# Kernel tuning notes

Hardware: AMD Instinct MI355X
Metric: run time of the kernel (lower is better)

Reference implementation:

```python
import jax, jax.numpy as jnp
import numpy as np

S, N, F = 32, 512, 256        # systems, atoms per system, feature/charge channels
R_EXCL = 5.0                  # neighbor_list_options.cutoff -> exclusion_radius
BOX = 30.0                    # box edge for random positions (Angstrom-scale)


def setup_inputs() -> dict:
    key = jax.random.key(0)
    k1, k2, k3, k4 = jax.random.split(key, 4)
    positions = jax.random.uniform(k1, (S, N, 3), dtype=jnp.float32) * BOX
    features = jax.random.normal(k2, (S * N, F), dtype=jnp.float32)
    W = jax.random.normal(k3, (F, F), dtype=jnp.float32) / jnp.sqrt(F)
    b = jax.random.normal(k4, (F,), dtype=jnp.float32) * 0.01
    return {"positions": positions, "features": features, "W": W, "b": b}


def _pair_potential(d):
    # CoulombPotential(smearing=None, exclusion_radius=R_EXCL).from_dist:
    # v(r) = (1/r) * (1 - f_cut(r)),  f_cut = 0.5*(1 + cos(pi*r/R_EXCL)) for r < R_EXCL
    fcut = jnp.where(d < R_EXCL, 0.5 * (1.0 + jnp.cos(jnp.pi * d / R_EXCL)), 0.0)
    return (1.0 / d) * (1.0 - fcut)


def reference(positions, features, W, b):
    # charges_map: Linear(F, F)
    charges = features @ W.T + b                      # [S*N, F]
    q = charges.reshape(S, N, F)                      # per-system charges

    # all-pairs distances per system (torch.combinations path, both directions
    # accumulated by the half-neighbor-list Calculator)
    diff = positions[:, :, None, :] - positions[:, None, :, :]   # [S,N,N,3]
    d = jnp.sqrt(jnp.sum(diff * diff, axis=-1))                  # [S,N,N]
    eye = jnp.eye(N, dtype=bool)
    d_safe = jnp.where(eye, 1.0, d)
    v = jnp.where(eye, 0.0, _pair_potential(d_safe))             # [S,N,N]

    # V_i = 0.5 * sum_j v(r_ij) q_j  (torchpme energy convention E = sum_i q_i V_i)
    V = 0.5 * jnp.einsum('sij,sjf->sif', v, q)                   # [S,N,F]

    # module returns potential * charges, concatenated over systems
    return (V * q).reshape(S * N, F)
```

## Files before the change

kernel.cpp:

```cpp
#include <hip/hip_runtime.h>
#include <hip/hip_cooperative_groups.h>

#define SY 32
#define NA 512
#define FD 256

typedef __attribute__((ext_vector_type(8))) short bf16x8;
typedef __attribute__((ext_vector_type(4))) short bf16x4;
typedef __attribute__((ext_vector_type(4))) float f32x4;

static __device__ __forceinline__ short f2bf(float x) {
    union { float f; unsigned u; } v; v.f = x;
    unsigned r = v.u + 0x7fffu + ((v.u >> 16) & 1u);
    return (short)(r >> 16);
}
static __device__ __forceinline__ float bf2f(short x) {
    union { float f; unsigned u; } v;
    v.u = ((unsigned)(unsigned short)x) << 16;
    return v.f;
}

static __device__ __forceinline__ void gld16(const void* g, void* l) {
    __builtin_amdgcn_global_load_lds(
        (const __attribute__((address_space(1))) void*)g,
        (__attribute__((address_space(3))) void*)l,
        16, 0, 0);
}

__global__ __launch_bounds__(256, 2) void charges_v2(
    const float* __restrict__ feat, const float* __restrict__ W,
    const float* __restrict__ b, short* __restrict__ qT)
{
    __shared__ __attribute__((aligned(16))) short sA[32 * 72];
    __shared__ __attribute__((aligned(16))) short sB[256 * 72];
    short* tr = sB;
    const int t    = threadIdx.x;
    const int i0   = blockIdx.x * 32;
    const int w    = t >> 6;
    const int lane = t & 63;
    const int n16  = lane & 15;
    const int quad = lane >> 4;

    f32x4 acc[2][4];
    #pragma unroll
    for (int a = 0; a < 2; ++a)
        #pragma unroll
        for (int c = 0; c < 4; ++c) acc[a][c] = (f32x4)0.0f;

    for (int k0 = 0; k0 < FD; k0 += 64) {
        #pragma unroll
        for (int m = 0; m < 2; ++m) {
            int lin = t + 256 * m;
            int i = lin >> 4, kq = lin & 15;
            float4 v = *(const float4*)&feat[(size_t)(i0 + i) * FD + k0 + 4 * kq];
            bf16x4 p; p[0] = f2bf(v.x); p[1] = f2bf(v.y);
                      p[2] = f2bf(v.z); p[3] = f2bf(v.w);
            *(bf16x4*)&sA[i * 72 + 4 * kq] = p;
        }
        #pragma unroll
        for (int m = 0; m < 16; ++m) {
            int lin = t + 256 * m;
            int f = lin >> 4, kq = lin & 15;
            float4 v = *(const float4*)&W[(size_t)f * FD + k0 + 4 * kq];
            bf16x4 p; p[0] = f2bf(v.x); p[1] = f2bf(v.y);
                      p[2] = f2bf(v.z); p[3] = f2bf(v.w);
            *(bf16x4*)&sB[f * 72 + 4 * kq] = p;
        }
        __syncthreads();

        #pragma unroll
        for (int ks = 0; ks < 64; ks += 32) {
            bf16x8 af[2], bfr[4];
            #pragma unroll
            for (int it = 0; it < 2; ++it)
                af[it] = *(const bf16x8*)&sA[(16 * it + n16) * 72 + ks + quad * 8];
            #pragma unroll
            for (int fb = 0; fb < 4; ++fb)
                bfr[fb] = *(const bf16x8*)&sB[(64 * w + 16 * fb + n16) * 72 + ks + quad * 8];
            __builtin_amdgcn_s_setprio(1);
            #pragma unroll
            for (int it = 0; it < 2; ++it)
                #pragma unroll
                for (int fb = 0; fb < 4; ++fb)
                    acc[it][fb] = __builtin_amdgcn_mfma_f32_16x16x32_bf16(
                        af[it], bfr[fb], acc[it][fb], 0, 0, 0);
            __builtin_amdgcn_s_setprio(0);
        }
        __syncthreads();
    }

    float bias[4];
    #pragma unroll
    for (int fb = 0; fb < 4; ++fb) bias[fb] = b[64 * w + 16 * fb + n16];

    #pragma unroll
    for (int it = 0; it < 2; ++it)
        #pragma unroll
        for (int fb = 0; fb < 4; ++fb) {
            bf16x4 p;
            #pragma unroll
            for (int r = 0; r < 4; ++r) p[r] = f2bf(acc[it][fb][r] + bias[fb]);
            int f = 64 * w + 16 * fb + n16;
            *(bf16x4*)&tr[f * 40 + 16 * it + 4 * quad] = p;
        }
    __syncthreads();
    {
        short* qTs = qT + ((size_t)(i0 >> 9)) * FD * NA;
        const int ilb = i0 & 511;
        #pragma unroll
        for (int n = 0; n < 4; ++n) {
            int S = n * 256 + t;
            int f = S >> 2;
            int c = S & 3;
            uint4 v = *(const uint4*)&tr[f * 40 + c * 8];
            *(uint4*)&qTs[(size_t)f * NA + ilb + c * 8] = v;
        }
    }
}

__global__ __launch_bounds__(256, 2) void lr_fast(
    const float* __restrict__ pos, float* __restrict__ gbuf,
    const short* __restrict__ qT)
{
    __shared__ float px[NA], py[NA], pz[NA];
    __shared__ __attribute__((aligned(16))) short sqb[FD * 128];
    __shared__ __attribute__((aligned(16))) short svb[32 * 128];

    const int blk = blockIdx.x;
    const int s   = blk & 31;
    const int i0  = (blk >> 5) * 32;
    const int t   = threadIdx.x;
    const int w    = t >> 6;
    const int lane = t & 63;
    const int n16  = lane & 15;
    const int quad = lane >> 4;

    for (int m = t; m < NA; m += 256) {
        const float* p = &pos[((size_t)s * NA + m) * 3];
        px[m] = p[0]; py[m] = p[1]; pz[m] = p[2];
    }

    f32x4 acc[2][4];
    #pragma unroll
    for (int a = 0; a < 2; ++a)
        #pragma unroll
        for (int c = 0; c < 4; ++c) acc[a][c] = (f32x4)0.0f;
    float qreg[2][4][4];

    const short* qTs = qT + (size_t)s * FD * NA;
    const int pi = t & 31;
    const int pc = t >> 5;
    const int gi = i0 + pi;
    const int wbase = t & ~63;

    __syncthreads();
    const float xi = px[gi], yi = py[gi], zi = pz[gi];

    for (int j0 = 0; j0 < NA; j0 += 128) {
        #pragma unroll
        for (int n = 0; n < 16; ++n) {
            int Sl = n * 256 + t;
            int f  = Sl >> 4;
            int cs = Sl & 15;
            int c  = (cs - f) & 15;
            gld16(&qTs[(size_t)f * NA + j0 + c * 8],
                  &sqb[(n * 256 + wbase) * 8]);
        }
        bf16x8 vA, vB;
        #pragma unroll
        for (int jj = 0; jj < 8; ++jj) {
            int gj = j0 + pc * 16 + jj;
            float dx = xi - px[gj];
            float dy = yi - py[gj];
            float dz = zi - pz[gj];
            float r2 = dx * dx + dy * dy + dz * dz;
            float inv = __builtin_amdgcn_rsqf(r2);
            float dd  = r2 * inv;
            float sn = __sinf(dd * 0.31415926535f);
            float om = (dd < 5.0f) ? sn * sn : 1.0f;
            float vv = (gi != gj) ? 0.5f * om * inv : 0.0f;
            vA[jj] = f2bf(vv);
        }
        #pragma unroll
        for (int jj = 0; jj < 8; ++jj) {
            int gj = j0 + pc * 16 + 8 + jj;
            float dx = xi - px[gj];
            float dy = yi - py[gj];
            float dz = zi - pz[gj];
            float r2 = dx * dx + dy * dy + dz * dz;
            float inv = __builtin_amdgcn_rsqf(r2);
            float dd  = r2 * inv;
            float sn = __sinf(dd * 0.31415926535f);
            float om = (dd < 5.0f) ? sn * sn : 1.0f;
            float vv = (gi != gj) ? 0.5f * om * inv : 0.0f;
            vB[jj] = f2bf(vv);
        }
        *(bf16x8*)&svb[pi * 128 + (((2 * pc + pi) & 15) * 8)]     = vA;
        *(bf16x8*)&svb[pi * 128 + (((2 * pc + 1 + pi) & 15) * 8)] = vB;
        __syncthreads();

        if (j0 == (i0 & ~127)) {
            const int jb0 = i0 & 127;
            #pragma unroll
            for (int it = 0; it < 2; ++it)
                #pragma unroll
                for (int fb = 0; fb < 4; ++fb) {
                    int f = 64 * w + 16 * fb + n16;
                    #pragma unroll
                    for (int r = 0; r < 4; ++r) {
                        int jl = jb0 + 16 * it + 4 * quad + r;
                        int c  = jl >> 3, o = jl & 7;
                        qreg[it][fb][r] =
                            bf2f(sqb[f * 128 + (((c + f) & 15) * 8) + o]);
                    }
                }
        }

        #pragma unroll
        for (int kh = 0; kh < 4; ++kh) {
            const int c = kh * 4 + quad;
            bf16x8 a0 = *(const bf16x8*)&svb[n16 * 128 + (((c + n16) & 15) * 8)];
            bf16x8 a1 = *(const bf16x8*)&svb[(16 + n16) * 128 + (((c + 16 + n16) & 15) * 8)];
            bf16x8 bq[4];
            #pragma unroll
            for (int fb = 0; fb < 4; ++fb) {
                int f = 64 * w + 16 * fb + n16;
                bq[fb] = *(const bf16x8*)&sqb[f * 128 + (((c + f) & 15) * 8)];
            }
            __builtin_amdgcn_s_setprio(1);
            #pragma unroll
            for (int fb = 0; fb < 4; ++fb) {
                acc[0][fb] = __builtin_amdgcn_mfma_f32_16x16x32_bf16(
                    a0, bq[fb], acc[0][fb], 0, 0, 0);
                acc[1][fb] = __builtin_amdgcn_mfma_f32_16x16x32_bf16(
                    a1, bq[fb], acc[1][fb], 0, 0, 0);
            }
            __builtin_amdgcn_s_setprio(0);
        }
        __syncthreads();
    }

    #pragma unroll
    for (int it = 0; it < 2; ++it)
        #pragma unroll
        for (int fb = 0; fb < 4; ++fb)
            #pragma unroll
            for (int r = 0; r < 4; ++r) {
                int i = i0 + 16 * it + 4 * quad + r;
                int f = 64 * w + 16 * fb + n16;
                size_t a = ((size_t)s * NA + i) * FD + f;
                gbuf[a] = acc[it][fb][r] * qreg[it][fb][r];
            }
}

__global__ __launch_bounds__(512) void charges_mfma(
    const float* __restrict__ feat, const float* __restrict__ W,
    const float* __restrict__ b, float* __restrict__ qfp,
    short* __restrict__ qT)
{
    __shared__ __attribute__((aligned(16))) short sA[64 * 72];
    __shared__ __attribute__((aligned(16))) short sB[256 * 72];
    __shared__ __attribute__((aligned(16))) short tr[256 * 72];
    const int t    = threadIdx.x;
    const int i0   = blockIdx.x * 64;
    const int w    = t >> 6;
    const int lane = t & 63;
    const int n16  = lane & 15;
    const int quad = lane >> 4;

    f32x4 acc[4][2];
    #pragma unroll
    for (int a = 0; a < 4; ++a)
        #pragma unroll
        for (int c = 0; c < 2; ++c) acc[a][c] = (f32x4)0.0f;

    for (int k0 = 0; k0 < FD; k0 += 64) {
        #pragma unroll
        for (int m = 0; m < 2; ++m) {
            int lin = t + 512 * m;
            int i = lin >> 4, kq = lin & 15;
            float4 v = *(const float4*)&feat[(size_t)(i0 + i) * FD + k0 + 4 * kq];
            bf16x4 p; p[0] = f2bf(v.x); p[1] = f2bf(v.y);
                      p[2] = f2bf(v.z); p[3] = f2bf(v.w);
            *(bf16x4*)&sA[i * 72 + 4 * kq] = p;
        }
        #pragma unroll
        for (int m = 0; m < 8; ++m) {
            int lin = t + 512 * m;
            int f = lin >> 4, kq = lin & 15;
            float4 v = *(const float4*)&W[(size_t)f * FD + k0 + 4 * kq];
            bf16x4 p; p[0] = f2bf(v.x); p[1] = f2bf(v.y);
                      p[2] = f2bf(v.z); p[3] = f2bf(v.w);
            *(bf16x4*)&sB[f * 72 + 4 * kq] = p;
        }
        __syncthreads();

        #pragma unroll
        for (int ks = 0; ks < 64; ks += 32) {
            bf16x8 af[4], bfr[2];
            #pragma unroll
            for (int it = 0; it < 4; ++it)
                af[it] = *(const bf16x8*)&sA[(16 * it + n16) * 72 + ks + quad * 8];
            #pragma unroll
            for (int fb = 0; fb < 2; ++fb)
                bfr[fb] = *(const bf16x8*)&sB[(32 * w + 16 * fb + n16) * 72 + ks + quad * 8];
            #pragma unroll
            for (int it = 0; it < 4; ++it)
                #pragma unroll
                for (int fb = 0; fb < 2; ++fb)
                    acc[it][fb] = __builtin_amdgcn_mfma_f32_16x16x32_bf16(
                        af[it], bfr[fb], acc[it][fb], 0, 0, 0);
        }
        __syncthreads();
    }

    float bias[2];
    #pragma unroll
    for (int fb = 0; fb < 2; ++fb) bias[fb] = b[32 * w + 16 * fb + n16];

    if (qfp) {
        #pragma unroll
        for (int it = 0; it < 4; ++it)
            #pragma unroll
            for (int fb = 0; fb < 2; ++fb)
                #pragma unroll
                for (int r = 0; r < 4; ++r) {
                    int i = i0 + 16 * it + 4 * quad + r;
                    int f = 32 * w + 16 * fb + n16;
                    qfp[(size_t)i * FD + f] = acc[it][fb][r] + bias[fb];
                }
    }

    #pragma unroll
    for (int it = 0; it < 4; ++it)
        #pragma unroll
        for (int fb = 0; fb < 2; ++fb) {
            bf16x4 p;
            #pragma unroll
            for (int r = 0; r < 4; ++r) p[r] = f2bf(acc[it][fb][r] + bias[fb]);
            int f = 32 * w + 16 * fb + n16;
            *(bf16x4*)&tr[f * 72 + 16 * it + 4 * quad] = p;
        }
    __syncthreads();
    {
        short* qTs = qT + ((size_t)(i0 >> 9)) * FD * NA;
        const int ilb = i0 & 511;
        #pragma unroll
        for (int n = 0; n < 4; ++n) {
            int S = n * 512 + t;
            int f = S >> 3;
            int c = S & 7;
            uint4 v = *(const uint4*)&tr[f * 72 + c * 8];
            *(uint4*)&qTs[(size_t)f * NA + ilb + c * 8] = v;
        }
    }
}

__global__ __launch_bounds__(256) void lr_coop(
    const float* __restrict__ pos, float* __restrict__ gbuf)
{
    __shared__ float px[NA], py[NA], pz[NA];
    __shared__ __attribute__((aligned(16))) short svb[64 * 40];
    __shared__ __attribute__((aligned(16))) short sqb[FD * 40];

    const int blk = blockIdx.x;
    const int s   = blk & 31;
    const int i0  = (blk >> 5) * 64;
    const int t   = threadIdx.x;
    const int w    = t >> 6;
    const int lane = t & 63;
    const int n16  = lane & 15;
    const int quad = lane >> 4;

    for (int m = t; m < NA; m += 256) {
        const float* p = &pos[((size_t)s * NA + m) * 3];
        px[m] = p[0]; py[m] = p[1]; pz[m] = p[2];
    }

    f32x4 acc[4][4];
    #pragma unroll
    for (int a = 0; a < 4; ++a)
        #pragma unroll
        for (int c = 0; c < 4; ++c) acc[a][c] = (f32x4)0.0f;

    __syncthreads();

    const int fq  = t >> 2;
    const int jb  = t & 3;
    const int iv  = t & 63;
    const int jbv = t >> 6;
    const int gi  = i0 + iv;

    float4 rq[8];
    #pragma unroll
    for (int m = 0; m < 8; ++m)
        rq[m] = *(const float4*)&gbuf[((size_t)s * NA + 8 * jb + m) * FD + 4 * fq];

    for (int j0 = 0; j0 < NA; j0 += 32) {
        bf16x8 vrow;
        #pragma unroll
        for (int jj = 0; jj < 8; ++jj) {
            int gj = j0 + 8 * jbv + jj;
            float dx = px[gi] - px[gj];
            float dy = py[gi] - py[gj];
            float dz = pz[gi] - pz[gj];
            float dd = sqrtf(dx * dx + dy * dy + dz * dz);
            float om = (dd < 5.0f) ? 0.5f * (1.0f - __cosf(dd * 0.62831853071795f))
                                   : 1.0f;
            float vv = (gi != gj) ? (0.5f * om * __builtin_amdgcn_rcpf(dd)) : 0.0f;
            vrow[jj] = f2bf(vv);
        }
        bf16x8 rows[4];
        #pragma unroll
        for (int m = 0; m < 8; ++m) {
            rows[0][m] = f2bf(rq[m].x);
            rows[1][m] = f2bf(rq[m].y);
            rows[2][m] = f2bf(rq[m].z);
            rows[3][m] = f2bf(rq[m].w);
        }
        #pragma unroll
        for (int d = 0; d < 4; ++d) {
            int f = 4 * fq + d;
            int phys = (jb + (f >> 3)) & 3;
            *(bf16x8*)&sqb[f * 40 + phys * 8] = rows[d];
        }
        {
            int phys = (jbv + (iv >> 3)) & 3;
            *(bf16x8*)&svb[iv * 40 + phys * 8] = vrow;
        }
        {
            int jn = (j0 + 32) & (NA - 1);
            #pragma unroll
            for (int m = 0; m < 8; ++m)
                rq[m] = *(const float4*)&gbuf[((size_t)s * NA + jn + 8 * jb + m) * FD + 4 * fq];
        }
        __syncthreads();

        bf16x8 af[4], bfr[4];
        #pragma unroll
        for (int it = 0; it < 4; ++it) {
            int i = 16 * it + n16;
            int phys = (quad + (i >> 3)) & 3;
            af[it] = *(const bf16x8*)&svb[i * 40 + phys * 8];
        }
        #pragma unroll
        for (int fb = 0; fb < 4; ++fb) {
            int f = 16 * (4 * w + fb) + n16;
            int phys = (quad + (f >> 3)) & 3;
            bfr[fb] = *(const bf16x8*)&sqb[f * 40 + phys * 8];
        }
        #pragma unroll
        for (int it = 0; it < 4; ++it)
            #pragma unroll
            for (int fb = 0; fb < 4; ++fb)
                acc[it][fb] = __builtin_amdgcn_mfma_f32_16x16x32_bf16(
                    af[it], bfr[fb], acc[it][fb], 0, 0, 0);
        __syncthreads();
    }

    cooperative_groups::this_grid().sync();

    #pragma unroll
    for (int it = 0; it < 4; ++it)
        #pragma unroll
        for (int fb = 0; fb < 4; ++fb)
            #pragma unroll
            for (int r = 0; r < 4; ++r) {
                int i = i0 + 16 * it + 4 * quad + r;
                int f = 16 * (4 * w + fb) + n16;
                size_t a = ((size_t)s * NA + i) * FD + f;
                gbuf[a] = acc[it][fb][r] * gbuf[a];
            }
}

extern "C" void kernel_launch(void* const* d_in, const int* in_sizes, int n_in,
                              void* d_out, int out_size, void* d_ws, size_t ws_size,
                              hipStream_t stream) {
    const float* positions = (const float*)d_in[0];
    const float* features  = (const float*)d_in[1];
    const float* W         = (const float*)d_in[2];
    const float* b         = (const float*)d_in[3];
    float* gbuf = (float*)d_out;

    const size_t qT_bytes = (size_t)SY * NA * FD * sizeof(short);
    const bool fast = (ws_size >= qT_bytes);
    short* qT = fast ? (short*)d_ws : nullptr;

    if (fast) {
        charges_v2<<<dim3(512), 256, 0, stream>>>(features, W, b, qT);
        lr_fast<<<dim3(512), 256, 0, stream>>>(positions, gbuf, qT);
    } else {
        charges_mfma<<<dim3(256), 512, 0, stream>>>(features, W, b, gbuf,
                                                    (short*)d_out );
        void* args[] = {(void*)&positions, (void*)&gbuf};
        hipLaunchCooperativeKernel((void*)lr_coop, dim3(256), dim3(256),
                                   args, 0, stream);
    }
}
```

Measured before the change: 96.47 us.

## Load GEMM B-operands directly from global memory and double-buffer LDS tiles

```diff
diff --git a/kernel.cpp b/kernel.cpp
--- a/kernel.cpp
+++ b/kernel.cpp
@@ -20,20 +20,12 @@
     return v.f;
 }
 
-static __device__ __forceinline__ void gld16(const void* g, void* l) {
-    __builtin_amdgcn_global_load_lds(
-        (const __attribute__((address_space(1))) void*)g,
-        (__attribute__((address_space(3))) void*)l,
-        16, 0, 0);
-}
-
 __global__ __launch_bounds__(256, 2) void charges_v2(
     const float* __restrict__ feat, const float* __restrict__ W,
     const float* __restrict__ b, short* __restrict__ qT)
 {
-    __shared__ __attribute__((aligned(16))) short sA[32 * 72];
-    __shared__ __attribute__((aligned(16))) short sB[256 * 72];
-    short* tr = sB;
+    __shared__ __attribute__((aligned(16))) short sA[2][32 * 72];
+    __shared__ __attribute__((aligned(16))) short tr[256 * 40];
     const int t    = threadIdx.x;
     const int i0   = blockIdx.x * 32;
     const int w    = t >> 6;
@@ -47,6 +39,7 @@
         #pragma unroll
         for (int c = 0; c < 4; ++c) acc[a][c] = (f32x4)0.0f;
 
+    int cur = 0;
     for (int k0 = 0; k0 < FD; k0 += 64) {
         #pragma unroll
         for (int m = 0; m < 2; ++m) {
@@ -55,28 +48,30 @@
             float4 v = *(const float4*)&feat[(size_t)(i0 + i) * FD + k0 + 4 * kq];
             bf16x4 p; p[0] = f2bf(v.x); p[1] = f2bf(v.y);
                       p[2] = f2bf(v.z); p[3] = f2bf(v.w);
-            *(bf16x4*)&sA[i * 72 + 4 * kq] = p;
-        }
-        #pragma unroll
-        for (int m = 0; m < 16; ++m) {
-            int lin = t + 256 * m;
-            int f = lin >> 4, kq = lin & 15;
-            float4 v = *(const float4*)&W[(size_t)f * FD + k0 + 4 * kq];
-            bf16x4 p; p[0] = f2bf(v.x); p[1] = f2bf(v.y);
-                      p[2] = f2bf(v.z); p[3] = f2bf(v.w);
-            *(bf16x4*)&sB[f * 72 + 4 * kq] = p;
+            *(bf16x4*)&sA[cur][i * 72 + 4 * kq] = p;
         }
         __syncthreads();
 
         #pragma unroll
         for (int ks = 0; ks < 64; ks += 32) {
-            bf16x8 af[2], bfr[4];
+            bf16x8 af[2];
             #pragma unroll
             for (int it = 0; it < 2; ++it)
-                af[it] = *(const bf16x8*)&sA[(16 * it + n16) * 72 + ks + quad * 8];
-            #pragma unroll
-            for (int fb = 0; fb < 4; ++fb)
-                bfr[fb] = *(const bf16x8*)&sB[(64 * w + 16 * fb + n16) * 72 + ks + quad * 8];
+                af[it] = *(const bf16x8*)&sA[cur][(16 * it + n16) * 72 + ks + quad * 8];
+            bf16x8 bfr[4];
+            #pragma unroll
+            for (int fb = 0; fb < 4; ++fb) {
+                const float* wp = &W[(size_t)(64 * w + 16 * fb + n16) * FD
+                                     + k0 + ks + quad * 8];
+                float4 w0 = *(const float4*)wp;
+                float4 w1 = *(const float4*)(wp + 4);
+                bf16x8 p;
+                p[0] = f2bf(w0.x); p[1] = f2bf(w0.y);
+                p[2] = f2bf(w0.z); p[3] = f2bf(w0.w);
+                p[4] = f2bf(w1.x); p[5] = f2bf(w1.y);
+                p[6] = f2bf(w1.z); p[7] = f2bf(w1.w);
+                bfr[fb] = p;
+            }
             __builtin_amdgcn_s_setprio(1);
             #pragma unroll
             for (int it = 0; it < 2; ++it)
@@ -86,7 +81,7 @@
                         af[it], bfr[fb], acc[it][fb], 0, 0, 0);
             __builtin_amdgcn_s_setprio(0);
         }
-        __syncthreads();
+        cur ^= 1;
     }
 
     float bias[4];
@@ -123,8 +118,7 @@
     const short* __restrict__ qT)
 {
     __shared__ float px[NA], py[NA], pz[NA];
-    __shared__ __attribute__((aligned(16))) short sqb[FD * 128];
-    __shared__ __attribute__((aligned(16))) short svb[32 * 128];
+    __shared__ __attribute__((aligned(16))) short svb[2][32 * 128];
 
     const int blk = blockIdx.x;
     const int s   = blk & 31;
@@ -145,27 +139,29 @@
     for (int a = 0; a < 2; ++a)
         #pragma unroll
         for (int c = 0; c < 4; ++c) acc[a][c] = (f32x4)0.0f;
+
+    const short* qTs = qT + (size_t)s * FD * NA;
+
     float qreg[2][4][4];
-
-    const short* qTs = qT + (size_t)s * FD * NA;
+    #pragma unroll
+    for (int it = 0; it < 2; ++it)
+        #pragma unroll
+        for (int fb = 0; fb < 4; ++fb) {
+            int f = 64 * w + 16 * fb + n16;
+            bf16x4 qv = *(const bf16x4*)&qTs[(size_t)f * NA + i0 + 16 * it + 4 * quad];
+            #pragma unroll
+            for (int r = 0; r < 4; ++r) qreg[it][fb][r] = bf2f(qv[r]);
+        }
+
     const int pi = t & 31;
     const int pc = t >> 5;
     const int gi = i0 + pi;
-    const int wbase = t & ~63;
 
     __syncthreads();
     const float xi = px[gi], yi = py[gi], zi = pz[gi];
 
+    int cur = 0;
     for (int j0 = 0; j0 < NA; j0 += 128) {
-        #pragma unroll
-        for (int n = 0; n < 16; ++n) {
-            int Sl = n * 256 + t;
-            int f  = Sl >> 4;
-            int cs = Sl & 15;
-            int c  = (cs - f) & 15;
-            gld16(&qTs[(size_t)f * NA + j0 + c * 8],
-                  &sqb[(n * 256 + wbase) * 8]);
-        }
         bf16x8 vA, vB;
         #pragma unroll
         for (int jj = 0; jj < 8; ++jj) {
@@ -195,37 +191,20 @@
             float vv = (gi != gj) ? 0.5f * om * inv : 0.0f;
             vB[jj] = f2bf(vv);
         }
-        *(bf16x8*)&svb[pi * 128 + (((2 * pc + pi) & 15) * 8)]     = vA;
-        *(bf16x8*)&svb[pi * 128 + (((2 * pc + 1 + pi) & 15) * 8)] = vB;
-        __syncthreads();
-
-        if (j0 == (i0 & ~127)) {
-            const int jb0 = i0 & 127;
-            #pragma unroll
-            for (int it = 0; it < 2; ++it)
-                #pragma unroll
-                for (int fb = 0; fb < 4; ++fb) {
-                    int f = 64 * w + 16 * fb + n16;
-                    #pragma unroll
-                    for (int r = 0; r < 4; ++r) {
-                        int jl = jb0 + 16 * it + 4 * quad + r;
-                        int c  = jl >> 3, o = jl & 7;
-                        qreg[it][fb][r] =
-                            bf2f(sqb[f * 128 + (((c + f) & 15) * 8) + o]);
-                    }
-                }
-        }
+        *(bf16x8*)&svb[cur][pi * 128 + (((2 * pc + pi) & 15) * 8)]     = vA;
+        *(bf16x8*)&svb[cur][pi * 128 + (((2 * pc + 1 + pi) & 15) * 8)] = vB;
+        __syncthreads();
 
         #pragma unroll
         for (int kh = 0; kh < 4; ++kh) {
             const int c = kh * 4 + quad;
-            bf16x8 a0 = *(const bf16x8*)&svb[n16 * 128 + (((c + n16) & 15) * 8)];
-            bf16x8 a1 = *(const bf16x8*)&svb[(16 + n16) * 128 + (((c + 16 + n16) & 15) * 8)];
+            bf16x8 a0 = *(const bf16x8*)&svb[cur][n16 * 128 + (((c + n16) & 15) * 8)];
+            bf16x8 a1 = *(const bf16x8*)&svb[cur][(16 + n16) * 128 + (((c + 16 + n16) & 15) * 8)];
             bf16x8 bq[4];
             #pragma unroll
             for (int fb = 0; fb < 4; ++fb) {
                 int f = 64 * w + 16 * fb + n16;
-                bq[fb] = *(const bf16x8*)&sqb[f * 128 + (((c + f) & 15) * 8)];
+                bq[fb] = *(const bf16x8*)&qTs[(size_t)f * NA + j0 + c * 8];
             }
             __builtin_amdgcn_s_setprio(1);
             #pragma unroll
@@ -237,7 +216,7 @@
             }
             __builtin_amdgcn_s_setprio(0);
         }
-        __syncthreads();
+        cur ^= 1;
     }
 
     #pragma unroll
```

New measurement: 110.7 us. 1.15x slower.
